# Kernel optimization log

Hardware: AMD Instinct MI355X
Metric: run time of the kernel (lower is better)

## Reference

```python
import jax, jax.numpy as jnp
import numpy as np
from jax import lax

TAU = 2.0          # spikingjelly LIFNode default tau
VTH = 1.0          # v_threshold
ALPHA = 2.0        # ATan surrogate alpha (grad only; fwd is heaviside)
N_WIN = (2, 4, 4)
TOPK = 4
HEADS = 8
EPS = 1e-5


@jax.custom_vjp
def spike(x):
    return (x >= 0).astype(x.dtype)

def _spike_fwd(x):
    return (x >= 0).astype(x.dtype), x

def _spike_bwd(x, g):
    sg = (ALPHA / 2.0) / (1.0 + (jnp.pi / 2.0 * ALPHA * x) ** 2)
    return (g * sg,)

spike.defvjp(_spike_fwd, _spike_bwd)


def lif(x_seq):
    # multi-step LIF, v_reset=None (soft reset), decay_input=True, detach_reset
    def step(v, x):
        v = v + (x - v) / TAU
        s = spike(v - VTH)
        v = v - lax.stop_gradient(s) * VTH
        return v, s
    v0 = jnp.zeros_like(x_seq[0])
    _, s_seq = lax.scan(step, v0, x_seq)
    return s_seq


def bn3d(x, g, b):
    # track_running_stats=False -> always batch stats; step_mode 'm' folds T into batch.
    # x: [T,B,C,Lt,Lh,Lw]; normalize per-channel over (T,B,Lt,Lh,Lw)
    ax = (0, 1, 3, 4, 5)
    m = x.mean(ax, keepdims=True)
    v = x.var(ax, keepdims=True)
    sh = (1, 1, -1, 1, 1, 1)
    return g.reshape(sh) * (x - m) * lax.rsqrt(v + EPS) + b.reshape(sh)


def bra(x, wqkv, bqkv, lepe_w, wo, bo):
    # Bi-level routing attention over 3D windows. x: [N, Lt, Lh, Lw, C]
    N, Lt, Lh, Lw, C = x.shape
    nt, nh, nw = N_WIN
    rt, rh, rw = Lt // nt, Lh // nh, Lw // nw
    R, P = nt * nh * nw, rt * rh * rw
    Dh = C // HEADS

    qkv = x @ wqkv + bqkv                       # [N,Lt,Lh,Lw,3C]
    q, k, v = jnp.split(qkv, 3, axis=-1)

    def to_reg(t):  # -> [N, R, P, C]
        t = t.reshape(N, nt, rt, nh, rh, nw, rw, C)
        return t.transpose(0, 1, 3, 5, 2, 4, 6, 7).reshape(N, R, P, C)

    def from_reg(t):  # [N,R,P,C] -> [N,Lt,Lh,Lw,C]
        t = t.reshape(N, nt, nh, nw, rt, rh, rw, C)
        return t.transpose(0, 1, 4, 2, 5, 3, 6, 7).reshape(N, Lt, Lh, Lw, C)

    qr, kr, vr = to_reg(q), to_reg(k), to_reg(v)

    # coarse routing: region means, top-k region selection
    a_r = jnp.einsum('nrc,nsc->nrs', qr.mean(2), kr.mean(2))   # [N,R,R]
    _, idx = lax.top_k(a_r, TOPK)                               # [N,R,TOPK]

    # gather selected regions' k,v: [N,R,TOPK,P,C] -> [N,R,TOPK*P,H,Dh]
    kg = jax.vmap(lambda a, i: a[i])(kr, idx)
    vg = jax.vmap(lambda a, i: a[i])(vr, idx)
    kg = kg.reshape(N, R, TOPK * P, HEADS, Dh)
    vg = vg.reshape(N, R, TOPK * P, HEADS, Dh)
    qh = qr.reshape(N, R, P, HEADS, Dh)

    logits = jnp.einsum('nrphd,nrkhd->nrhpk', qh * (Dh ** -0.5), kg)
    attn = jax.nn.softmax(logits, axis=-1)
    out = jnp.einsum('nrhpk,nrkhd->nrphd', attn, vg).reshape(N, R, P, C)
    out = from_reg(out)

    # LEPE: depthwise 3x3x3 conv on v
    v_ncdhw = v.transpose(0, 4, 1, 2, 3)
    lepe = lax.conv_general_dilated(
        v_ncdhw, lepe_w, (1, 1, 1), 'SAME', feature_group_count=C,
        dimension_numbers=('NCDHW', 'OIDHW', 'NCDHW'))
    out = out + lepe.transpose(0, 2, 3, 4, 1)

    return out @ wo + bo


def setup_inputs() -> dict:
    key = jax.random.key(0)
    ks = jax.random.split(key, 8)
    T, B, C, Lt, Lh, Lw = 2, 1, 256, 8, 32, 32
    inp = {
        'x': jax.random.normal(ks[0], (T, B, C, Lt, Lh, Lw), jnp.float32),
        'bn1_g': jnp.ones((C,), jnp.float32),
        'bn1_b': jnp.zeros((C,), jnp.float32),
        'wqkv': jax.random.normal(ks[1], (C, 3 * C), jnp.float32) * (C ** -0.5),
        'bqkv': jnp.zeros((3 * C,), jnp.float32),
        'lepe_w': jax.random.normal(ks[2], (C, 1, 3, 3, 3), jnp.float32) * 0.1,
        'wo': jax.random.normal(ks[3], (C, C), jnp.float32) * (C ** -0.5),
        'bo': jnp.zeros((C,), jnp.float32),
        'bn2_g': jnp.ones((C,), jnp.float32),
        'bn2_b': jnp.zeros((C,), jnp.float32),
        'ffn_w1': jax.random.normal(ks[4], (C, 4 * C), jnp.float32) * (C ** -0.5),
        'ffn_b1': jnp.zeros((4 * C,), jnp.float32),
        'ffn_w2': jax.random.normal(ks[5], (4 * C, C), jnp.float32) * ((4 * C) ** -0.5),
        'ffn_b2': jnp.zeros((C,), jnp.float32),
        'scale': jnp.ones((1,), jnp.float32) * 0.5,
    }
    return inp


def reference(x, bn1_g, bn1_b, wqkv, bqkv, lepe_w, wo, bo,
              bn2_g, bn2_b, ffn_w1, ffn_b1, ffn_w2, ffn_b2, scale):
    T, B, C, Lt, Lh, Lw = x.shape

    # --- attention branch ---
    s1 = lif(bn3d(x, bn1_g, bn1_b))                       # [T,B,C,Lt,Lh,Lw]
    sa = s1.transpose(0, 1, 3, 4, 5, 2).reshape(T * B, Lt, Lh, Lw, C)
    a = bra(sa, wqkv, bqkv, lepe_w, wo, bo)
    a = a.reshape(T, B, Lt, Lh, Lw, C).transpose(0, 1, 5, 2, 3, 4)
    x = x + a * scale

    # --- FFN branch (1x1x1 conv = channel GEMM) ---
    s2 = lif(bn3d(x, bn2_g, bn2_b))
    h = jax.nn.gelu(jnp.einsum('tbcdhw,cf->tbfdhw', s2, ffn_w1)
                    + ffn_b1.reshape(1, 1, -1, 1, 1, 1), approximate=False)
    f = (jnp.einsum('tbfdhw,fc->tbcdhw', h, ffn_w2)
         + ffn_b2.reshape(1, 1, -1, 1, 1, 1))
    return x + f * scale
```

## Files before the change

kernel.cpp:

```cpp
#include <hip/hip_runtime.h>
#include <math.h>

#define CC 256
#define LL 8192
#define RR 32
#define PPP 256
#define NTOP 4
#define TOKS 16384
#define TBLK (TOKS * 32)

typedef unsigned short u16;
typedef __attribute__((ext_vector_type(8))) short short8;
typedef __attribute__((ext_vector_type(8))) unsigned short u16x8;
typedef __attribute__((ext_vector_type(4))) float f32x4;
typedef __attribute__((ext_vector_type(4))) unsigned short u16x4;

#if defined(__has_builtin)
#if __has_builtin(__builtin_amdgcn_exp2f)
#define EXP2(x) __builtin_amdgcn_exp2f(x)
#endif
#endif
#ifndef EXP2
#define EXP2(x) exp2f(x)
#endif

__device__ inline u16 f2bf(float f) {
  unsigned int b = __float_as_uint(f);
  unsigned int r = (b + 0x7FFFu + ((b >> 16) & 1u)) >> 16;
  return (u16)r;
}
__device__ inline float bf2f(u16 x) { return __uint_as_float(((unsigned int)x) << 16); }

__global__ __launch_bounds__(256) void k_bnstats(const float* __restrict__ x,
                                                 float* __restrict__ mean,
                                                 float* __restrict__ istd) {
  int c = blockIdx.x, tid = threadIdx.x;
  float s = 0.f, sq = 0.f;
  for (int i = tid; i < 2 * LL / 4; i += 256) {
    int t = i >> 11, l4 = (i & 2047) * 4;
    float4 v = *(const float4*)&x[(size_t)(t * CC + c) * LL + l4];
    s += (v.x + v.y) + (v.z + v.w);
    sq += (v.x * v.x + v.y * v.y) + (v.z * v.z + v.w * v.w);
  }
  __shared__ float rs[256], rq[256];
  rs[tid] = s; rq[tid] = sq;
  __syncthreads();
  for (int off = 128; off > 0; off >>= 1) {
    if (tid < off) { rs[tid] += rs[tid + off]; rq[tid] += rq[tid + off]; }
    __syncthreads();
  }
  if (tid == 0) {
    float m = rs[0] * (1.f / (2 * LL));
    float var = rq[0] * (1.f / (2 * LL)) - m * m;
    mean[c] = m;
    istd[c] = rsqrtf(var + 1e-5f);
  }
}

__global__ __launch_bounds__(256) void k_lifT(const float* __restrict__ xin,
                                              const float* __restrict__ mean,
                                              const float* __restrict__ istd,
                                              const float* __restrict__ g,
                                              const float* __restrict__ b,
                                              u16* __restrict__ actT) {
  __shared__ float t0[32][33], t1[32][33];
  int l0 = blockIdx.x * 32, c0 = blockIdx.y * 32;
  int tx = threadIdx.x & 31, ty = threadIdx.x >> 5;
  for (int i = 0; i < 32; i += 8) {
    int c = c0 + ty + i;
    float m = mean[c], is = istd[c], gg = g[c], bb = b[c];
    float x0 = xin[(size_t)c * LL + l0 + tx];
    float x1 = xin[(size_t)(CC + c) * LL + l0 + tx];
    float y0 = gg * (x0 - m) * is + bb;
    float y1 = gg * (x1 - m) * is + bb;
    float v = y0 * 0.5f;
    float s0 = (v >= 1.f) ? 1.f : 0.f;
    v -= s0;
    v += (y1 - v) * 0.5f;
    float s1 = (v >= 1.f) ? 1.f : 0.f;
    t0[ty + i][tx] = s0;
    t1[ty + i][tx] = s1;
  }
  __syncthreads();
  size_t kb = (size_t)(c0 >> 5) * TBLK;
  for (int i = 0; i < 32; i += 8) {
    int l = l0 + ty + i;
    actT[kb + (size_t)l * 32 + tx] = f2bf(t0[tx][ty + i]);
    actT[kb + (size_t)(LL + l) * 32 + tx] = f2bf(t1[tx][ty + i]);
  }
}

__global__ __launch_bounds__(256) void k_tr(const float* __restrict__ in, u16* __restrict__ out,
                                            int R, int C) {
  __shared__ float t[32][33];
  int c0 = blockIdx.x * 32, r0 = blockIdx.y * 32;
  int tx = threadIdx.x & 31, ty = threadIdx.x >> 5;
  for (int i = 0; i < 32; i += 8)
    t[ty + i][tx] = in[(size_t)(r0 + ty + i) * C + c0 + tx];
  __syncthreads();
  size_t kb = (size_t)(r0 >> 5) * C * 32;
  for (int i = 0; i < 32; i += 8)
    out[kb + (size_t)(c0 + ty + i) * 32 + tx] = f2bf(t[tx][ty + i]);
}

__global__ __launch_bounds__(256) void k_trw(const float* __restrict__ w, float* __restrict__ wT) {
  int c = threadIdx.x;
  for (int tap = 0; tap < 27; ++tap) wT[tap * 256 + c] = w[c * 27 + tap];
}

template<int MR, int NR, int WCN>
__device__ inline void mfma_core_blk(const u16* __restrict__ A0, int sAb,
                                     const u16* __restrict__ B0, int sBb,
                                     int K, f32x4 acc[MR][NR]) {
  int lane = threadIdx.x & 63;
  int w = threadIdx.x >> 6;
  int wr = w / WCN, wc = w % WCN;
  int u = lane & 15;
  int g8 = (lane >> 4) * 8;
  const u16* Ap = A0 + (wr * MR * 16 + u) * 32 + g8;
  const u16* Bp = B0 + (wc * NR * 16 + u) * 32 + g8;
  for (int kb = 0; kb < (K >> 5); ++kb) {
    short8 af[MR], bfr[NR];
#pragma unroll
    for (int i = 0; i < MR; ++i)
      af[i] = *(const short8*)(Ap + (size_t)kb * sAb + i * 512);
#pragma unroll
    for (int j = 0; j < NR; ++j)
      bfr[j] = *(const short8*)(Bp + (size_t)kb * sBb + j * 512);
#pragma unroll
    for (int i = 0; i < MR; ++i)
#pragma unroll
      for (int j = 0; j < NR; ++j)
        acc[i][j] = __builtin_amdgcn_mfma_f32_16x16x32_bf16(af[i], bfr[j], acc[i][j], 0, 0, 0);
  }
}

__global__ __launch_bounds__(256) void k_gqkv(const u16* __restrict__ spkT, const u16* __restrict__ wT,
                                              const float* __restrict__ bias,
                                              u16* __restrict__ qh, u16* __restrict__ kh,
                                              u16* __restrict__ vt, u16* __restrict__ vtok) {
  f32x4 acc[4][4] = {};
  int n0 = blockIdx.x * 128, m0 = blockIdx.y * 128;
  mfma_core_blk<4, 4, 2>(spkT + (size_t)m0 * 32, TBLK, wT + (size_t)n0 * 32, 768 * 32, 256, acc);
  int lane = threadIdx.x & 63, w = threadIdx.x >> 6;
  int wr = w >> 1, wc = w & 1;
  int u = lane & 15;
  const float QSC = 0.255034865f;
#pragma unroll
  for (int i = 0; i < 4; ++i) {
#pragma unroll
    for (int reg = 0; reg < 4; ++reg) {
      int token = m0 + wr * 64 + i * 16 + (lane >> 4) * 4 + reg;
      int l = token & (LL - 1), nb = token >> 13;
      int lt = l >> 10, lh = (l >> 5) & 31, lw = l & 31;
      int r = ((lt >> 2) * 4 + (lh >> 3)) * 4 + (lw >> 3);
      int p = ((lt & 3) * 8 + (lh & 7)) * 8 + (lw & 7);
      int nr = nb * RR + r;
#pragma unroll
      for (int j = 0; j < 4; ++j) {
        int ch = n0 + wc * 64 + j * 16 + u;
        float val = acc[i][j][reg] + bias[ch];
        int which = ch >> 8, c = ch & 255;
        int hh = c >> 5, dh = c & 31;
        size_t hb = ((size_t)nr * 8 + hh) * 8192;
        if (which == 0) {
          qh[hb + p * 32 + dh] = f2bf(val * QSC);
        } else if (which == 1) {
          kh[hb + p * 32 + dh] = f2bf(val);
        } else {
          u16 vb = f2bf(val);
          vt[hb + dh * 256 + p] = vb;
          vtok[(size_t)token * CC + c] = vb;
        }
      }
    }
  }
}

__global__ __launch_bounds__(256) void k_means(const u16* __restrict__ qh, const u16* __restrict__ kh,
                                               float* __restrict__ qm, float* __restrict__ km) {
  int nrh = blockIdx.x;
  int nr = nrh >> 3, h = nrh & 7;
  int tid = threadIdx.x;
  int dh = tid & 31, pg = tid >> 5;
  size_t base = (size_t)nrh * 8192;
  float sq = 0.f, sk = 0.f;
  for (int p = pg * 32; p < pg * 32 + 32; ++p) {
    sq += bf2f(qh[base + p * 32 + dh]);
    sk += bf2f(kh[base + p * 32 + dh]);
  }
  __shared__ float rq[256], rk[256];
  rq[tid] = sq; rk[tid] = sk;
  __syncthreads();
  if (pg == 0) {
#pragma unroll
    for (int g = 1; g < 8; ++g) { sq += rq[g * 32 + dh]; sk += rk[g * 32 + dh]; }
    qm[nr * 256 + h * 32 + dh] = sq * (1.f / 256);
    km[nr * 256 + h * 32 + dh] = sk * (1.f / 256);
  }
}

__global__ __launch_bounds__(256) void k_route(const float* __restrict__ qm,
                                               const float* __restrict__ km,
                                               int* __restrict__ idx) {
  int nr = blockIdx.x;
  int n = nr >> 5;
  int tid = threadIdx.x;
  int s = tid >> 3, cg = tid & 7;
  const float* qrow = qm + nr * CC;
  const float* krow = km + (n * RR + s) * CC;
  float sum = 0.f;
  for (int c = cg * 32; c < cg * 32 + 32; ++c) sum += qrow[c] * krow[c];
  sum += __shfl_xor(sum, 1);
  sum += __shfl_xor(sum, 2);
  sum += __shfl_xor(sum, 4);
  __shared__ float ar[32];
  if (cg == 0) ar[s] = sum;
  __syncthreads();
  if (tid == 0) {
    for (int t = 0; t < NTOP; ++t) {
      float best = -1e30f; int bi = 0;
      for (int ss = 0; ss < 32; ++ss)
        if (ar[ss] > best) { best = ar[ss]; bi = ss; }
      ar[bi] = -1e30f;
      idx[nr * NTOP + t] = bi;
    }
  }
}

__global__ __launch_bounds__(256) void k_attn_mfma(const u16* __restrict__ qh,
                                                   const u16* __restrict__ kh,
                                                   const u16* __restrict__ vt,
                                                   const int* __restrict__ idx,
                                                   u16* __restrict__ oreg) {
  int h = blockIdx.x, r = blockIdx.y, n = blockIdx.z;
  int nr = n * RR + r;
  int lane = threadIdx.x & 63;
  int w = threadIdx.x >> 6;
  int u = lane & 15, g = lane >> 4;
  int swz = (u >> 1) & 3;
  __shared__ __align__(16) unsigned pl[4096];
  unsigned* plw = &pl[w * 1024];

  const u16* qb = qh + ((size_t)nr * 8 + h) * 8192;
  int q0 = w * 64;
  short8 qf[4];
#pragma unroll
  for (int f = 0; f < 4; ++f)
    qf[f] = *(const short8*)(qb + (size_t)(q0 + f * 16 + u) * 32 + g * 8);

  f32x4 accO[2][4] = {};
  float lsum[4] = {0.f, 0.f, 0.f, 0.f};
  const int* idxp = &idx[nr * NTOP];

  for (int ri = 0; ri < NTOP; ++ri) {
    int reg = idxp[ri];
    size_t rb = ((size_t)(n * RR + reg) * 8 + h) * 8192;
#pragma unroll 2
    for (int t = 0; t < 8; ++t) {
      int pb = t * 32;
      short8 kf0 = *(const short8*)(kh + rb + (size_t)(pb + u) * 32 + g * 8);
      short8 kf1 = *(const short8*)(kh + rb + (size_t)(pb + 16 + u) * 32 + g * 8);
      short8 vf0 = *(const short8*)(vt + rb + (size_t)u * 256 + pb + g * 8);
      short8 vf1 = *(const short8*)(vt + rb + (size_t)(16 + u) * 256 + pb + g * 8);

      f32x4 s0[4], s1[4];
      __builtin_amdgcn_s_setprio(1);
#pragma unroll
      for (int nf = 0; nf < 4; ++nf) {
        s0[nf] = __builtin_amdgcn_mfma_f32_16x16x32_bf16(kf0, qf[nf], (f32x4){0.f, 0.f, 0.f, 0.f}, 0, 0, 0);
        s1[nf] = __builtin_amdgcn_mfma_f32_16x16x32_bf16(kf1, qf[nf], (f32x4){0.f, 0.f, 0.f, 0.f}, 0, 0, 0);
      }
      __builtin_amdgcn_s_setprio(0);
#pragma unroll
      for (int nf = 0; nf < 4; ++nf) {
#pragma unroll
        for (int mf = 0; mf < 2; ++mf) {
          f32x4 sv = mf ? s1[nf] : s0[nf];
          float p0 = EXP2(sv[0]);
          float p1 = EXP2(sv[1]);
          float p2 = EXP2(sv[2]);
          float p3 = EXP2(sv[3]);
          lsum[nf] += (p0 + p1) + (p2 + p3);
          unsigned wA, wB;
          asm("v_cvt_pk_bf16_f32 %0, %1, %2" : "=v"(wA) : "v"(p0), "v"(p1));
          asm("v_cvt_pk_bf16_f32 %0, %1, %2" : "=v"(wB) : "v"(p2), "v"(p3));
          int bidx = (mf * 2 + (g >> 1)) ^ swz;
          *(uint2*)&plw[nf * 256 + u * 16 + bidx * 4 + (g & 1) * 2] = make_uint2(wA, wB);
        }
      }
      __builtin_amdgcn_s_setprio(1);
#pragma unroll
      for (int nf = 0; nf < 4; ++nf) {
        short8 pf = *(const short8*)&plw[nf * 256 + u * 16 + ((g ^ swz) << 2)];
        accO[0][nf] = __builtin_amdgcn_mfma_f32_16x16x32_bf16(vf0, pf, accO[0][nf], 0, 0, 0);
        accO[1][nf] = __builtin_amdgcn_mfma_f32_16x16x32_bf16(vf1, pf, accO[1][nf], 0, 0, 0);
      }
      __builtin_amdgcn_s_setprio(0);
    }
  }

#pragma unroll
  for (int nf = 0; nf < 4; ++nf) {
    lsum[nf] += __shfl_xor(lsum[nf], 16);
    lsum[nf] += __shfl_xor(lsum[nf], 32);
    float inv = 1.f / lsum[nf];
    int q = q0 + nf * 16 + u;
    int z = (((r >> 4) & 1) << 2) | ((q >> 6) & 3);
    int y = (((r >> 2) & 3) << 3) | ((q >> 3) & 7);
    int xx = ((r & 3) << 3) | (q & 7);
    int l = (z << 10) | (y << 5) | xx;
    u16* ob = &oreg[((size_t)(n * LL + l)) * CC + h * 32];
#pragma unroll
    for (int mf = 0; mf < 2; ++mf) {
      f32x4 o = mf ? accO[1][nf] : accO[0][nf];
      float a0 = o[0] * inv, a1 = o[1] * inv, a2 = o[2] * inv, a3 = o[3] * inv;
      unsigned w0, w1;
      asm("v_cvt_pk_bf16_f32 %0, %1, %2" : "=v"(w0) : "v"(a0), "v"(a1));
      asm("v_cvt_pk_bf16_f32 %0, %1, %2" : "=v"(w1) : "v"(a2), "v"(a3));
      *(uint2*)&ob[mf * 16 + g * 4] = make_uint2(w0, w1);
    }
  }
}

__global__ __launch_bounds__(256) void k_lepe(const u16* __restrict__ oreg,
                                              const u16* __restrict__ vtok,
                                              const float* __restrict__ wT,
                                              u16* __restrict__ otok) {
  int vox = threadIdx.x >> 6;
  int b = blockIdx.x * 4 + vox;
  int l = b & (LL - 1);
  int lt = l >> 10, lh = (l >> 5) & 31, lw = l & 31;
  int c4 = (threadIdx.x & 63) * 4;
  const u16* vb = vtok + (size_t)b * CC + c4;
  float lx = 0.f, ly = 0.f, lz = 0.f, lww = 0.f;
#pragma unroll
  for (int dz = -1; dz <= 1; ++dz) {
#pragma unroll
    for (int dy = -1; dy <= 1; ++dy) {
#pragma unroll
      for (int dx = -1; dx <= 1; ++dx) {
        int z = lt + dz, y = lh + dy, xx = lw + dx;
        if (z >= 0 && z < 8 && y >= 0 && y < 32 && xx >= 0 && xx < 32) {
          int tap = ((dz + 1) * 3 + (dy + 1)) * 3 + (dx + 1);
          long off = (long)(dz * 1024 + dy * 32 + dx) * CC;
          float4 w4 = *(const float4*)&wT[tap * 256 + c4];
          u16x4 v4 = *(const u16x4*)&vb[off];
          lx = fmaf(w4.x, bf2f(v4[0]), lx);
          ly = fmaf(w4.y, bf2f(v4[1]), ly);
          lz = fmaf(w4.z, bf2f(v4[2]), lz);
          lww = fmaf(w4.w, bf2f(v4[3]), lww);
        }
      }
    }
  }
  u16x4 a4 = *(const u16x4*)&oreg[(size_t)b * CC + c4];
  size_t oaddr = (size_t)(c4 >> 5) * TBLK + (size_t)b * 32 + (c4 & 31);
  *(u16x4*)&otok[oaddr] =
      (u16x4){f2bf(bf2f(a4[0]) + lx), f2bf(bf2f(a4[1]) + ly),
              f2bf(bf2f(a4[2]) + lz), f2bf(bf2f(a4[3]) + lww)};
}

__global__ __launch_bounds__(256) void k_gffn1(const u16* __restrict__ sT, const u16* __restrict__ wT,
                                               const float* __restrict__ bias, u16* __restrict__ hbuf) {
  f32x4 acc[4][4] = {};
  int n0 = blockIdx.x * 128, m0 = blockIdx.y * 128;
  mfma_core_blk<4, 4, 2>(sT + (size_t)m0 * 32, TBLK, wT + (size_t)n0 * 32, 1024 * 32, 256, acc);
  int lane = threadIdx.x & 63, w = threadIdx.x >> 6;
  int wr = w >> 1, wc = w & 1;
#pragma unroll
  for (int i = 0; i < 4; ++i) {
#pragma unroll
    for (int reg = 0; reg < 4; ++reg) {
      int token = m0 + wr * 64 + i * 16 + (lane >> 4) * 4 + reg;
#pragma unroll
      for (int j = 0; j < 4; ++j) {
        int ch = n0 + wc * 64 + j * 16 + (lane & 15);
        float z = acc[i][j][reg] + bias[ch];
        float gel = 0.5f * z * (1.f + erff(z * 0.70710678118654752f));
        hbuf[(size_t)(ch >> 5) * TBLK + (size_t)token * 32 + (ch & 31)] = f2bf(gel);
      }
    }
  }
}

__global__ __launch_bounds__(128) void k_gffn2(const u16* __restrict__ w2T, const u16* __restrict__ hb,
                                               const float* __restrict__ bias, const float* __restrict__ scale,
                                               float* __restrict__ out) {
  f32x4 acc[2][4] = {};
  int n0 = blockIdx.x * 128, m0 = blockIdx.y * 32;
  mfma_core_blk<2, 4, 2>(w2T + (size_t)m0 * 32, 256 * 32, hb + (size_t)n0 * 32, TBLK, 1024, acc);
  int lane = threadIdx.x & 63, wc = threadIdx.x >> 6;
  float sc = scale[0];
#pragma unroll
  for (int i = 0; i < 2; ++i) {
#pragma unroll
    for (int reg = 0; reg < 4; ++reg) {
      int ch = m0 + i * 16 + (lane >> 4) * 4 + reg;
      float bb = bias[ch];
#pragma unroll
      for (int j = 0; j < 4; ++j) {
        int token = n0 + wc * 64 + j * 16 + (lane & 15);
        int t = token >> 13, l = token & (LL - 1);
        size_t oi = ((size_t)t * CC + ch) * LL + l;
        out[oi] += (acc[i][j][reg] + bb) * sc;
      }
    }
  }
}

__global__ __launch_bounds__(128) void k_gwo(const u16* __restrict__ woT, const u16* __restrict__ atok,
                                             const float* __restrict__ bias, const float* __restrict__ xin,
                                             const float* __restrict__ scale, float* __restrict__ out) {
  f32x4 acc[2][4] = {};
  int n0 = blockIdx.x * 128, m0 = blockIdx.y * 32;
  mfma_core_blk<2, 4, 2>(woT + (size_t)m0 * 32, 256 * 32, atok + (size_t)n0 * 32, TBLK, 256, acc);
  int lane = threadIdx.x & 63, wc = threadIdx.x >> 6;
  float sc = scale[0];
#pragma unroll
  for (int i = 0; i < 2; ++i) {
#pragma unroll
    for (int reg = 0; reg < 4; ++reg) {
      int ch = m0 + i * 16 + (lane >> 4) * 4 + reg;
      float bb = bias[ch];
#pragma unroll
      for (int j = 0; j < 4; ++j) {
        int token = n0 + wc * 64 + j * 16 + (lane & 15);
        int t = token >> 13, l = token & (LL - 1);
        size_t oi = ((size_t)t * CC + ch) * LL + l;
        out[oi] = xin[oi] + (acc[i][j][reg] + bb) * sc;
      }
    }
  }
}

extern "C" void kernel_launch(void* const* d_in, const int* in_sizes, int n_in,
                              void* d_out, int out_size, void* d_ws, size_t ws_size,
                              hipStream_t stream) {
  const float* x      = (const float*)d_in[0];
  const float* bn1_g  = (const float*)d_in[1];
  const float* bn1_b  = (const float*)d_in[2];
  const float* wqkv   = (const float*)d_in[3];
  const float* bqkv   = (const float*)d_in[4];
  const float* lepe_w = (const float*)d_in[5];
  const float* wo_w   = (const float*)d_in[6];
  const float* bo     = (const float*)d_in[7];
  const float* bn2_g  = (const float*)d_in[8];
  const float* bn2_b  = (const float*)d_in[9];
  const float* ffn_w1 = (const float*)d_in[10];
  const float* ffn_b1 = (const float*)d_in[11];
  const float* ffn_w2 = (const float*)d_in[12];
  const float* ffn_b2 = (const float*)d_in[13];
  const float* scale  = (const float*)d_in[14];
  float* out = (float*)d_out;

  float* ws    = (float*)d_ws;
  u16*   actT  = (u16*)(ws + 4194304);
  u16*   qhead = (u16*)(ws + 6291456);
  u16*   khead = (u16*)(ws + 8388608);
  u16*   vthead= (u16*)(ws + 10485760);
  u16*   vtok  = (u16*)(ws + 12582912);
  u16*   oreg  = (u16*)(ws + 16777216);
  u16*   hbuf  = (u16*)(ws + 6291456);
  u16*   wqkvT = (u16*)(ws + 20971520);
  u16*   w1T   = (u16*)(ws + 21069824);
  u16*   w2T   = (u16*)(ws + 21200896);
  u16*   woT   = (u16*)(ws + 21331968);
  float* sm    = ws + 21364736;
  float* mean1 = sm;
  float* istd1 = sm + 256;
  float* mean2 = sm + 512;
  float* istd2 = sm + 768;
  float* qm    = sm + 1024;
  float* km    = sm + 1024 + 16384;
  int*   idxb  = (int*)(sm + 1024 + 32768);
  float* wTlep = sm + 1024 + 32768 + 256;

  k_tr<<<dim3(24, 8, 1), 256, 0, stream>>>(wqkv, wqkvT, 256, 768);
  k_tr<<<dim3(32, 8, 1), 256, 0, stream>>>(ffn_w1, w1T, 256, 1024);
  k_tr<<<dim3(8, 32, 1), 256, 0, stream>>>(ffn_w2, w2T, 1024, 256);
  k_tr<<<dim3(8, 8, 1), 256, 0, stream>>>(wo_w, woT, 256, 256);
  k_trw<<<1, 256, 0, stream>>>(lepe_w, wTlep);

  k_bnstats<<<256, 256, 0, stream>>>(x, mean1, istd1);
  k_lifT<<<dim3(256, 8), 256, 0, stream>>>(x, mean1, istd1, bn1_g, bn1_b, actT);
  k_gqkv<<<dim3(6, 128), 256, 0, stream>>>(actT, wqkvT, bqkv, qhead, khead, vthead, vtok);
  k_means<<<512, 256, 0, stream>>>(qhead, khead, qm, km);
  k_route<<<64, 256, 0, stream>>>(qm, km, idxb);
  k_attn_mfma<<<dim3(8, RR, 2), 256, 0, stream>>>(qhead, khead, vthead, idxb, oreg);
  k_lepe<<<4096, 256, 0, stream>>>(oreg, vtok, wTlep, actT);
  k_gwo<<<dim3(128, 8), 128, 0, stream>>>(woT, actT, bo, x, scale, out);

  k_bnstats<<<256, 256, 0, stream>>>(out, mean2, istd2);
  k_lifT<<<dim3(256, 8), 256, 0, stream>>>(out, mean2, istd2, bn2_g, bn2_b, actT);
  k_gffn1<<<dim3(8, 128), 256, 0, stream>>>(actT, w1T, ffn_b1, hbuf);
  k_gffn2<<<dim3(128, 8), 128, 0, stream>>>(w2T, hbuf, ffn_b2, scale, out);
}
```

Before: 215.4 us.

## Fuse second BN statistics into Wo GEMM epilogue and swap GEMM grid order

The Wo projection epilogue now reduces per-channel sum and sum-of-squares of the residual output through wave shuffles and shared memory. It writes per-block partials, and a small finalize kernel turns them into mean and inverse std. This removes the separate k_bnstats pass that re-read the whole 16 MB output tensor. The QKV and FFN1 GEMM grids are also transposed so consecutive blocks walk token tiles while sharing one weight tile, which may improve L2 reuse. It costs extra shuffles and a sync in the Wo epilogue, and the single-pass variance keeps its float cancellation risk.

```diff
diff --git a/kernel.cpp b/kernel.cpp
--- a/kernel.cpp
+++ b/kernel.cpp
@@ -52,6 +52,28 @@
   if (tid == 0) {
     float m = rs[0] * (1.f / (2 * LL));
     float var = rq[0] * (1.f / (2 * LL)) - m * m;
+    mean[c] = m;
+    istd[c] = rsqrtf(var + 1e-5f);
+  }
+}
+
+__global__ __launch_bounds__(128) void k_bnfin(const float* __restrict__ psum,
+                                               const float* __restrict__ psq,
+                                               float* __restrict__ mean,
+                                               float* __restrict__ istd) {
+  int c = blockIdx.x;
+  int tid = threadIdx.x;
+  __shared__ float rs[128], rq[128];
+  rs[tid] = psum[c * 128 + tid];
+  rq[tid] = psq[c * 128 + tid];
+  __syncthreads();
+  for (int off = 64; off > 0; off >>= 1) {
+    if (tid < off) { rs[tid] += rs[tid + off]; rq[tid] += rq[tid + off]; }
+    __syncthreads();
+  }
+  if (tid == 0) {
+    float m = rs[0] * (1.f / 16384.f);
+    float var = rq[0] * (1.f / 16384.f) - m * m;
     mean[c] = m;
     istd[c] = rsqrtf(var + 1e-5f);
   }
@@ -140,7 +162,7 @@
                                               u16* __restrict__ qh, u16* __restrict__ kh,
                                               u16* __restrict__ vt, u16* __restrict__ vtok) {
   f32x4 acc[4][4] = {};
-  int n0 = blockIdx.x * 128, m0 = blockIdx.y * 128;
+  int m0 = blockIdx.x * 128, n0 = blockIdx.y * 128;
   mfma_core_blk<4, 4, 2>(spkT + (size_t)m0 * 32, TBLK, wT + (size_t)n0 * 32, 768 * 32, 256, acc);
   int lane = threadIdx.x & 63, w = threadIdx.x >> 6;
   int wr = w >> 1, wc = w & 1;
@@ -364,7 +386,7 @@
 __global__ __launch_bounds__(256) void k_gffn1(const u16* __restrict__ sT, const u16* __restrict__ wT,
                                                const float* __restrict__ bias, u16* __restrict__ hbuf) {
   f32x4 acc[4][4] = {};
-  int n0 = blockIdx.x * 128, m0 = blockIdx.y * 128;
+  int m0 = blockIdx.x * 128, n0 = blockIdx.y * 128;
   mfma_core_blk<4, 4, 2>(sT + (size_t)m0 * 32, TBLK, wT + (size_t)n0 * 32, 1024 * 32, 256, acc);
   int lane = threadIdx.x & 63, w = threadIdx.x >> 6;
   int wr = w >> 1, wc = w & 1;
@@ -411,26 +433,46 @@
 
 __global__ __launch_bounds__(128) void k_gwo(const u16* __restrict__ woT, const u16* __restrict__ atok,
                                              const float* __restrict__ bias, const float* __restrict__ xin,
-                                             const float* __restrict__ scale, float* __restrict__ out) {
+                                             const float* __restrict__ scale, float* __restrict__ out,
+                                             float* __restrict__ psum, float* __restrict__ psq) {
   f32x4 acc[2][4] = {};
   int n0 = blockIdx.x * 128, m0 = blockIdx.y * 32;
   mfma_core_blk<2, 4, 2>(woT + (size_t)m0 * 32, 256 * 32, atok + (size_t)n0 * 32, TBLK, 256, acc);
   int lane = threadIdx.x & 63, wc = threadIdx.x >> 6;
+  int g = lane >> 4;
   float sc = scale[0];
+  __shared__ float lsum[2][32], lsq[2][32];
 #pragma unroll
   for (int i = 0; i < 2; ++i) {
 #pragma unroll
     for (int reg = 0; reg < 4; ++reg) {
-      int ch = m0 + i * 16 + (lane >> 4) * 4 + reg;
+      int ch = m0 + i * 16 + g * 4 + reg;
       float bb = bias[ch];
+      float s = 0.f, q = 0.f;
 #pragma unroll
       for (int j = 0; j < 4; ++j) {
         int token = n0 + wc * 64 + j * 16 + (lane & 15);
         int t = token >> 13, l = token & (LL - 1);
         size_t oi = ((size_t)t * CC + ch) * LL + l;
-        out[oi] = xin[oi] + (acc[i][j][reg] + bb) * sc;
-      }
-    }
+        float v = xin[oi] + (acc[i][j][reg] + bb) * sc;
+        out[oi] = v;
+        s += v; q += v * v;
+      }
+      s += __shfl_xor(s, 1); q += __shfl_xor(q, 1);
+      s += __shfl_xor(s, 2); q += __shfl_xor(q, 2);
+      s += __shfl_xor(s, 4); q += __shfl_xor(q, 4);
+      s += __shfl_xor(s, 8); q += __shfl_xor(q, 8);
+      if ((lane & 15) == 0) {
+        lsum[wc][i * 16 + g * 4 + reg] = s;
+        lsq[wc][i * 16 + g * 4 + reg] = q;
+      }
+    }
+  }
+  __syncthreads();
+  int tid = threadIdx.x;
+  if (tid < 32) {
+    psum[(m0 + tid) * 128 + blockIdx.x] = lsum[0][tid] + lsum[1][tid];
+    psq[(m0 + tid) * 128 + blockIdx.x] = lsq[0][tid] + lsq[1][tid];
   }
 }
 
@@ -475,6 +517,8 @@
   float* km    = sm + 1024 + 16384;
   int*   idxb  = (int*)(sm + 1024 + 32768);
   float* wTlep = sm + 1024 + 32768 + 256;
+  float* psum  = sm + 1024 + 32768 + 256 + 6912;
+  float* psq   = psum + 32768;
 
   k_tr<<<dim3(24, 8, 1), 256, 0, stream>>>(wqkv, wqkvT, 256, 768);
   k_tr<<<dim3(32, 8, 1), 256, 0, stream>>>(ffn_w1, w1T, 256, 1024);
@@ -484,15 +528,15 @@
 
   k_bnstats<<<256, 256, 0, stream>>>(x, mean1, istd1);
   k_lifT<<<dim3(256, 8), 256, 0, stream>>>(x, mean1, istd1, bn1_g, bn1_b, actT);
-  k_gqkv<<<dim3(6, 128), 256, 0, stream>>>(actT, wqkvT, bqkv, qhead, khead, vthead, vtok);
+  k_gqkv<<<dim3(128, 6), 256, 0, stream>>>(actT, wqkvT, bqkv, qhead, khead, vthead, vtok);
   k_means<<<512, 256, 0, stream>>>(qhead, khead, qm, km);
   k_route<<<64, 256, 0, stream>>>(qm, km, idxb);
   k_attn_mfma<<<dim3(8, RR, 2), 256, 0, stream>>>(qhead, khead, vthead, idxb, oreg);
   k_lepe<<<4096, 256, 0, stream>>>(oreg, vtok, wTlep, actT);
-  k_gwo<<<dim3(128, 8), 128, 0, stream>>>(woT, actT, bo, x, scale, out);
-
-  k_bnstats<<<256, 256, 0, stream>>>(out, mean2, istd2);
+  k_gwo<<<dim3(128, 8), 128, 0, stream>>>(woT, actT, bo, x, scale, out, psum, psq);
+
+  k_bnfin<<<256, 128, 0, stream>>>(psum, psq, mean2, istd2);
   k_lifT<<<dim3(256, 8), 256, 0, stream>>>(out, mean2, istd2, bn2_g, bn2_b, actT);
-  k_gffn1<<<dim3(8, 128), 256, 0, stream>>>(actT, w1T, ffn_b1, hbuf);
+  k_gffn1<<<dim3(128, 8), 256, 0, stream>>>(actT, w1T, ffn_b1, hbuf);
   k_gffn2<<<dim3(128, 8), 128, 0, stream>>>(w2T, hbuf, ffn_b2, scale, out);
 }
```

New measurement: 212.7 us. Within noise of the previous version (-1.3%).
